# Performance work log

Measured on AMD Instinct MI355X. Metric: run time of the kernel, lower is better.

Reference implementation:

```python
import jax, jax.numpy as jnp
import numpy as np

N, NX, NQ, NU = 262144, 64, 64, 16
STD = 0.5


def setup_inputs() -> dict:
    key = jax.random.key(0)
    ks = jax.random.split(key, 8)
    x = jax.random.normal(ks[0], (N, NX), jnp.float32)
    u = jax.random.normal(ks[1], (N, NU), jnp.float32)
    A = jax.random.normal(ks[2], (NX, NX), jnp.float32) * STD
    B1 = jax.random.normal(ks[3], (NX, NQ), jnp.float32) * STD
    B2 = jax.random.normal(ks[4], (NX, NU), jnp.float32) * STD
    C1 = jax.random.normal(ks[5], (NQ, NX), jnp.float32) * STD
    # D11 is strictly lower triangular (forward substitution / triangular solve)
    D11 = jnp.tril(jax.random.normal(ks[6], (NQ, NQ), jnp.float32) * STD, -1)
    D12 = jax.random.normal(ks[7], (NQ, NU), jnp.float32) * STD
    bv = jnp.zeros((NQ,), jnp.float32)  # bias=False in original module
    bx = jnp.zeros((NX,), jnp.float32)
    return {"x": x, "u": u, "A": A, "B1": B1, "B2": B2,
            "C1": C1, "D11": D11, "D12": D12, "bv": bv, "bx": bx}


def _calculate_w(x, u, C1, D11, D12, bv):
    """Solve w = act(C1 x + D11 w + D12 u + bv) by forward substitution.
    D11 is strictly lower triangular, so row i of w only depends on rows < i."""
    act = jax.nn.relu
    nq = D11.shape[0]
    base = x @ C1.T + u @ D12.T + bv          # (N, nq): input-dependent part
    eye = jnp.eye(nq, dtype=x.dtype)           # one-hot rows for the scatter

    def step(w, inp):
        d_row, b_col, e = inp                  # (nq,), (N,), (nq,)
        v = b_col + w @ d_row                  # (N,)  uses only already-filled w cols
        w = w + act(v)[:, None] * e            # write column i (matches torch select_w)
        return w, None

    w0 = jnp.zeros((x.shape[0], nq), x.dtype)
    w, _ = jax.lax.scan(step, w0, (D11, base.T, eye))
    return w


def reference(x, u, A, B1, B2, C1, D11, D12, bv, bx):
    # x_dot = A x + B1 w + B2 u + bx
    w = _calculate_w(x, u, C1, D11, D12, bv)
    x_dot = x @ A.T + w @ B1.T + u @ B2.T + bx
    return x_dot
```

## Files before the change

kernel.cpp:

```cpp
#include <hip/hip_runtime.h>
#include <utility>

#define NROWS 262144
#define BT 512
#define RPB 128

typedef float f16v __attribute__((ext_vector_type(16)));


__global__ void prep_kernel(const float* __restrict__ A, const float* __restrict__ B1,
                            const float* __restrict__ B2, const float* __restrict__ C1,
                            const float* __restrict__ D11, const float* __restrict__ D12,
                            const float* __restrict__ bv, const float* __restrict__ bx,
                            float* __restrict__ ws) {
    int g = blockIdx.x * 256 + threadIdx.x;
    if (g < 4096) {
        int r = g >> 6, c = g & 63;
        int to = c * 64 + r;
        ws[0     + to] = C1[g];
        ws[4096  + to] = D11[g];
        ws[9280  + to] = A[g];
        ws[13376 + to] = B1[g];
    }
    if (g < 1024) {
        int r = g >> 4, c = g & 15;
        int to = c * 64 + r;
        ws[8192  + to] = D12[g];
        ws[17472 + to] = B2[g];
    }
    if (g < 64) {
        ws[9216  + g] = bv[g];
        ws[18496 + g] = bx[g];
    }
}

__device__ __forceinline__ f16v lds16(const float* p) { return *(const f16v*)p; }

template<int I>
__device__ __forceinline__ void substep(f16v& s, const float* D11s, int c16, int c) {
    const float v = s[I & 15];
    const int b = __builtin_amdgcn_ds_swizzle(__float_as_int(v), ((I >> 4) << 5) | 0x1C);
    const float wv = fmaxf(__int_as_float(b), 0.0f);
    s += lds16(D11s + I * 64 + c16) * wv;
    s[I & 15] = (c == (I >> 4)) ? wv : s[I & 15];
}

template<int... Is>
__device__ __forceinline__ void subst_all(f16v& s, const float* D11s, int c16, int c,
                                          std::integer_sequence<int, Is...>) {
    (substep<Is>(s, D11s, c16, c), ...);
}

__global__ __launch_bounds__(BT, 4) void renl2_fused(const float* __restrict__ x,
                                                     const float* __restrict__ u,
                                                     const float* __restrict__ ws,
                                                     float* out ) {
    __shared__ float sm[9280];
    const int tid = threadIdx.x;
    const int c   = tid & 3;
    const int c16 = c << 4;
    const int r   = tid >> 2;
    const int row = blockIdx.x * RPB + r;

    const float* __restrict__ xr = x + (size_t)row * 64;
    const float* __restrict__ ur = u + (size_t)row * 16;
    float* wr = out + (size_t)row * 64;

#pragma unroll 4
    for (int i = tid; i < 9280; i += BT) sm[i] = ws[i];
    __syncthreads();

    f16v s = lds16(sm + 9216 + c16);
#pragma unroll 1
    for (int j = 0; j < 64; j += 4) {
        const float4 xv = *(const float4*)(xr + j);
#pragma unroll
        for (int jj = 0; jj < 4; jj++) {
            const float xs = (jj == 0) ? xv.x : (jj == 1) ? xv.y : (jj == 2) ? xv.z : xv.w;
            s += lds16(sm + (j + jj) * 64 + c16) * xs;
        }
    }
    {
        const float4 uv0 = *(const float4*)(ur);
        const float4 uv1 = *(const float4*)(ur + 4);
        const float4 uv2 = *(const float4*)(ur + 8);
        const float4 uv3 = *(const float4*)(ur + 12);
        const float us[16] = {uv0.x,uv0.y,uv0.z,uv0.w, uv1.x,uv1.y,uv1.z,uv1.w,
                              uv2.x,uv2.y,uv2.z,uv2.w, uv3.x,uv3.y,uv3.z,uv3.w};
#pragma unroll
        for (int j = 0; j < 16; j++)
            s += lds16(sm + 8192 + j * 64 + c16) * us[j];
    }

    subst_all(s, sm + 4096, c16, c, std::make_integer_sequence<int, 64>{});

    *(float4*)(wr + c16)      = float4{s[0],  s[1],  s[2],  s[3]};
    *(float4*)(wr + c16 + 4)  = float4{s[4],  s[5],  s[6],  s[7]};
    *(float4*)(wr + c16 + 8)  = float4{s[8],  s[9],  s[10], s[11]};
    *(float4*)(wr + c16 + 12) = float4{s[12], s[13], s[14], s[15]};

    __syncthreads();
#pragma unroll 4
    for (int i = tid; i < 9280; i += BT) sm[i] = ws[9280 + i];
    __syncthreads();

    f16v acc = lds16(sm + 9216 + c16);
#pragma unroll 1
    for (int j = 0; j < 64; j += 4) {
        const float4 xv = *(const float4*)(xr + j);
#pragma unroll
        for (int jj = 0; jj < 4; jj++) {
            const float xs = (jj == 0) ? xv.x : (jj == 1) ? xv.y : (jj == 2) ? xv.z : xv.w;
            acc += lds16(sm + (j + jj) * 64 + c16) * xs;
        }
    }
    {
        const float4 uv0 = *(const float4*)(ur);
        const float4 uv1 = *(const float4*)(ur + 4);
        const float4 uv2 = *(const float4*)(ur + 8);
        const float4 uv3 = *(const float4*)(ur + 12);
        const float us[16] = {uv0.x,uv0.y,uv0.z,uv0.w, uv1.x,uv1.y,uv1.z,uv1.w,
                              uv2.x,uv2.y,uv2.z,uv2.w, uv3.x,uv3.y,uv3.z,uv3.w};
#pragma unroll
        for (int j = 0; j < 16; j++)
            acc += lds16(sm + 8192 + j * 64 + c16) * us[j];
    }
#pragma unroll 1
    for (int j = 0; j < 64; j += 4) {
        const float4 wv = *(const float4*)(wr + j);
#pragma unroll
        for (int jj = 0; jj < 4; jj++) {
            const float wsc = (jj == 0) ? wv.x : (jj == 1) ? wv.y : (jj == 2) ? wv.z : wv.w;
            acc += lds16(sm + 4096 + (j + jj) * 64 + c16) * wsc;
        }
    }

    *(float4*)(wr + c16)      = float4{acc[0],  acc[1],  acc[2],  acc[3]};
    *(float4*)(wr + c16 + 4)  = float4{acc[4],  acc[5],  acc[6],  acc[7]};
    *(float4*)(wr + c16 + 8)  = float4{acc[8],  acc[9],  acc[10], acc[11]};
    *(float4*)(wr + c16 + 12) = float4{acc[12], acc[13], acc[14], acc[15]};
}

extern "C" void kernel_launch(void* const* d_in, const int* in_sizes, int n_in,
                              void* d_out, int out_size, void* d_ws, size_t ws_size,
                              hipStream_t stream) {
    const float* x   = (const float*)d_in[0];
    const float* u   = (const float*)d_in[1];
    const float* A   = (const float*)d_in[2];
    const float* B1  = (const float*)d_in[3];
    const float* B2  = (const float*)d_in[4];
    const float* C1  = (const float*)d_in[5];
    const float* D11 = (const float*)d_in[6];
    const float* D12 = (const float*)d_in[7];
    const float* bv  = (const float*)d_in[8];
    const float* bx  = (const float*)d_in[9];
    float* out = (float*)d_out;
    float* ws  = (float*)d_ws;

    prep_kernel<<<16, 256, 0, stream>>>(A, B1, B2, C1, D11, D12, bv, bx, ws);
    renl2_fused<<<NROWS / RPB, BT, 0, stream>>>(x, u, ws, out);
}
```

Measured before the change: 286.6 us.

## Keep w in registers and broadcast via DPP instead of global round-trip

Stops writing the intermediate w to the output buffer and reading it back for the B1 product. w stays in registers and each element is broadcast across the four lanes of a quad with a DPP quad_perm move, replacing ds_swizzle in the triangular solve as well. This removes a 64-float-per-row global store and reload and uses a cheaper cross-lane op, at the cost of 64 extra DPP moves in the B1 pass and possibly higher register pressure.

```diff
diff --git a/kernel.cpp b/kernel.cpp
--- a/kernel.cpp
+++ b/kernel.cpp
@@ -36,11 +36,15 @@
 
 __device__ __forceinline__ f16v lds16(const float* p) { return *(const f16v*)p; }
 
+template<int Q>
+__device__ __forceinline__ float qbcast(float v) {
+    return __int_as_float(__builtin_amdgcn_update_dpp(
+        0, __float_as_int(v), Q * 0x55, 0xF, 0xF, true));
+}
+
 template<int I>
 __device__ __forceinline__ void substep(f16v& s, const float* D11s, int c16, int c) {
-    const float v = s[I & 15];
-    const int b = __builtin_amdgcn_ds_swizzle(__float_as_int(v), ((I >> 4) << 5) | 0x1C);
-    const float wv = fmaxf(__int_as_float(b), 0.0f);
+    const float wv = fmaxf(qbcast<(I >> 4)>(s[I & 15]), 0.0f);
     s += lds16(D11s + I * 64 + c16) * wv;
     s[I & 15] = (c == (I >> 4)) ? wv : s[I & 15];
 }
@@ -51,10 +55,21 @@
     (substep<Is>(s, D11s, c16, c), ...);
 }
 
+template<int J>
+__device__ __forceinline__ void b1step(f16v& acc, const f16v& w, const float* B1s, int c16) {
+    acc += lds16(B1s + J * 64 + c16) * qbcast<(J >> 4)>(w[J & 15]);
+}
+
+template<int... Js>
+__device__ __forceinline__ void b1_all(f16v& acc, const f16v& w, const float* B1s, int c16,
+                                       std::integer_sequence<int, Js...>) {
+    (b1step<Js>(acc, w, B1s, c16), ...);
+}
+
 __global__ __launch_bounds__(BT, 4) void renl2_fused(const float* __restrict__ x,
                                                      const float* __restrict__ u,
                                                      const float* __restrict__ ws,
-                                                     float* out ) {
+                                                     float* __restrict__ out) {
     __shared__ float sm[9280];
     const int tid = threadIdx.x;
     const int c   = tid & 3;
@@ -64,7 +79,6 @@
 
     const float* __restrict__ xr = x + (size_t)row * 64;
     const float* __restrict__ ur = u + (size_t)row * 16;
-    float* wr = out + (size_t)row * 64;
 
 #pragma unroll 4
     for (int i = tid; i < 9280; i += BT) sm[i] = ws[i];
@@ -94,17 +108,14 @@
 
     subst_all(s, sm + 4096, c16, c, std::make_integer_sequence<int, 64>{});
 
-    *(float4*)(wr + c16)      = float4{s[0],  s[1],  s[2],  s[3]};
-    *(float4*)(wr + c16 + 4)  = float4{s[4],  s[5],  s[6],  s[7]};
-    *(float4*)(wr + c16 + 8)  = float4{s[8],  s[9],  s[10], s[11]};
-    *(float4*)(wr + c16 + 12) = float4{s[12], s[13], s[14], s[15]};
-
     __syncthreads();
 #pragma unroll 4
     for (int i = tid; i < 9280; i += BT) sm[i] = ws[9280 + i];
     __syncthreads();
 
     f16v acc = lds16(sm + 9216 + c16);
+    b1_all(acc, s, sm + 4096, c16, std::make_integer_sequence<int, 64>{});
+
 #pragma unroll 1
     for (int j = 0; j < 64; j += 4) {
         const float4 xv = *(const float4*)(xr + j);
@@ -114,6 +125,7 @@
             acc += lds16(sm + (j + jj) * 64 + c16) * xs;
         }
     }
+
     {
         const float4 uv0 = *(const float4*)(ur);
         const float4 uv1 = *(const float4*)(ur + 4);
@@ -125,20 +137,12 @@
         for (int j = 0; j < 16; j++)
             acc += lds16(sm + 8192 + j * 64 + c16) * us[j];
     }
-#pragma unroll 1
-    for (int j = 0; j < 64; j += 4) {
-        const float4 wv = *(const float4*)(wr + j);
-#pragma unroll
-        for (int jj = 0; jj < 4; jj++) {
-            const float wsc = (jj == 0) ? wv.x : (jj == 1) ? wv.y : (jj == 2) ? wv.z : wv.w;
-            acc += lds16(sm + 4096 + (j + jj) * 64 + c16) * wsc;
-        }
-    }
 
-    *(float4*)(wr + c16)      = float4{acc[0],  acc[1],  acc[2],  acc[3]};
-    *(float4*)(wr + c16 + 4)  = float4{acc[4],  acc[5],  acc[6],  acc[7]};
-    *(float4*)(wr + c16 + 8)  = float4{acc[8],  acc[9],  acc[10], acc[11]};
-    *(float4*)(wr + c16 + 12) = float4{acc[12], acc[13], acc[14], acc[15]};
+    float* outr = out + (size_t)row * 64;
+    *(float4*)(outr + c16)      = float4{acc[0],  acc[1],  acc[2],  acc[3]};
+    *(float4*)(outr + c16 + 4)  = float4{acc[4],  acc[5],  acc[6],  acc[7]};
+    *(float4*)(outr + c16 + 8)  = float4{acc[8],  acc[9],  acc[10], acc[11]};
+    *(float4*)(outr + c16 + 12) = float4{acc[12], acc[13], acc[14], acc[15]};
 }
 
 extern "C" void kernel_launch(void* const* d_in, const int* in_sizes, int n_in,
```

Result: faster. 270.0 us (-5.8%).
